# Kernel tuning notes

Hardware: AMD Instinct MI355X
Metric: run time of the kernel (lower is better)

The kernel has to match this reference:

```python
import jax, jax.numpy as jnp
import numpy as np

M_MARGIN = 0.5
SCALE = 64.0
COS_M = float(np.cos(M_MARGIN))
SIN_M = float(np.sin(M_MARGIN))
TH = -COS_M
MM = SIN_M * M_MARGIN
NUM_CLASSES = 100000
IN_FEATURES = 512
BATCH = 512


def setup_inputs() -> dict:
    key = jax.random.key(0)
    k1, k2, k3 = jax.random.split(key, 3)
    x = jax.random.normal(k1, (BATCH, IN_FEATURES), dtype=jnp.float32)
    y = jax.random.randint(k2, (BATCH,), 0, NUM_CLASSES, dtype=jnp.int64 if jax.config.jax_enable_x64 else jnp.int32)
    # xavier_uniform-like init for weight [num_classes, in_features]
    limit = float(np.sqrt(6.0 / (NUM_CLASSES + IN_FEATURES)))
    weight = jax.random.uniform(k3, (NUM_CLASSES, IN_FEATURES), minval=-limit, maxval=limit, dtype=jnp.float32)
    return {"x": x, "y": y, "weight": weight}


def _l2_normalize(v, axis=-1, eps=1e-12):
    # matches F.normalize(p=2): v / max(||v||, eps)
    n = jnp.sqrt(jnp.sum(v * v, axis=axis, keepdims=True))
    return v / jnp.maximum(n, eps)


def reference(x, y, weight):
    # cosine logits: [B, C]
    xn = _l2_normalize(x)
    wn = _l2_normalize(weight)
    cos = jnp.einsum('bd,cd->bc', xn, wn)
    sin = jnp.sqrt(jnp.clip(1.0 - cos * cos, 0.0))
    cos_w_margin = cos * COS_M - sin * SIN_M
    cos_w_margin = jnp.where(cos > TH, cos_w_margin, cos - MM)
    ohe = jax.nn.one_hot(y, NUM_CLASSES, dtype=jnp.bool_)
    logit = jnp.where(ohe, cos_w_margin, cos) * SCALE
    # cross entropy, mean reduction
    logp = jax.nn.log_softmax(logit, axis=-1)
    nll = -jnp.take_along_axis(logp, y[:, None], axis=-1)[:, 0]
    return jnp.mean(nll)
```

## Files before the change

kernel.cpp:

```cpp
#include <hip/hip_runtime.h>
#include <hip/hip_bf16.h>
#include <cstdint>
#include <cstddef>

#define C_CLS   100000
#define D_FEAT  512
#define B_ROWS  512

#define COSM 0.8775825618903728f
#define SINM 0.479425538604203f
#define TH_  (-0.8775825618903728f)
#define MM_  0.2397127693021015f

typedef __bf16 bf16x8 __attribute__((ext_vector_type(8)));
typedef __bf16 bf16x4 __attribute__((ext_vector_type(4)));
typedef float  f32x4  __attribute__((ext_vector_type(4)));

typedef __attribute__((address_space(3))) void lds_void;
typedef const __attribute__((address_space(1))) void g_void;

__device__ __forceinline__ void async_copy16(const void* g, void* l) {
    __builtin_amdgcn_global_load_lds((g_void*)g, (lds_void*)l, 16, 0, 0);
}

__global__ void k_xnorm(const float* __restrict__ x, __bf16* __restrict__ xn,
                        float* __restrict__ row_sum, float* __restrict__ tlogit) {
    const int row  = blockIdx.x;
    const int lane = threadIdx.x;
    const f32x4* p = (const f32x4*)(x + (size_t)row * D_FEAT);
    f32x4 a = p[lane];
    f32x4 b = p[lane + 64];
    float s = a[0]*a[0] + a[1]*a[1] + a[2]*a[2] + a[3]*a[3]
            + b[0]*b[0] + b[1]*b[1] + b[2]*b[2] + b[3]*b[3];
    #pragma unroll
    for (int m = 32; m >= 1; m >>= 1) s += __shfl_xor(s, m, 64);
    const float inv = 1.0f / fmaxf(sqrtf(s), 1e-12f);
    bf16x4 o0 = { (__bf16)(a[0]*inv), (__bf16)(a[1]*inv), (__bf16)(a[2]*inv), (__bf16)(a[3]*inv) };
    bf16x4 o1 = { (__bf16)(b[0]*inv), (__bf16)(b[1]*inv), (__bf16)(b[2]*inv), (__bf16)(b[3]*inv) };
    *(bf16x4*)(xn + (size_t)row * D_FEAT + lane * 4)       = o0;
    *(bf16x4*)(xn + (size_t)row * D_FEAT + 256 + lane * 4) = o1;
    if (lane == 0) { row_sum[row] = 0.0f; tlogit[row] = 0.0f; }
}

__global__ void k_wnorm(const float* __restrict__ w, float* __restrict__ inv_wn) {
    const int row  = blockIdx.x * 4 + (threadIdx.x >> 6);
    const int lane = threadIdx.x & 63;
    if (row >= C_CLS) return;
    const f32x4* p = (const f32x4*)(w + (size_t)row * D_FEAT);
    f32x4 a = p[lane];
    f32x4 b = p[lane + 64];
    float s = a[0]*a[0] + a[1]*a[1] + a[2]*a[2] + a[3]*a[3]
            + b[0]*b[0] + b[1]*b[1] + b[2]*b[2] + b[3]*b[3];
    #pragma unroll
    for (int m = 32; m >= 1; m >>= 1) s += __shfl_xor(s, m, 64);
    if (lane == 0) inv_wn[row] = 1.0f / fmaxf(sqrtf(s), 1e-12f);
}

__global__ __launch_bounds__(256, 2) void k_gemm(
        const __bf16* __restrict__ xn, const float* __restrict__ w,
        const float* __restrict__ inv_wn, const int* __restrict__ y,
        float* __restrict__ row_sum, float* __restrict__ tlogit) {

    __shared__ __align__(16) __bf16 As[4 * 128 * 8];
    __shared__ __align__(16) float  Bs[4 * 128 * 8];
    __shared__ int ys[128];

    const int tid = threadIdx.x;
    const int bm  = blockIdx.x & 3;
    const int bn  = blockIdx.x >> 2;

    if (tid < 128) ys[tid] = y[bm * 128 + tid];

    const int wave = tid >> 6;
    const int lane = tid & 63;
    const int wm   = wave >> 1;
    const int wn   = wave & 1;
    const int quad = lane >> 4;
    const int l15  = lane & 15;

    f32x4 acc[4][4];
    #pragma unroll
    for (int i = 0; i < 4; ++i)
        #pragma unroll
        for (int j = 0; j < 4; ++j) acc[i][j] = (f32x4){0.f, 0.f, 0.f, 0.f};

    for (int kt = 0; kt < 16; ++kt) {
        const int k0 = kt * 32;
        #pragma unroll
        for (int i = 0; i < 2; ++i) {
            const int c  = tid + i * 256;
            const int qc = c >> 7, rc = c & 127;
            const __bf16* g = xn + (size_t)(bm * 128 + rc) * D_FEAT + k0 + qc * 8;
            async_copy16(g, &As[(size_t)c * 8]);
        }
        #pragma unroll
        for (int i = 0; i < 4; ++i) {
            const int c  = tid + i * 256;
            const int qc = c >> 8, rc = (c >> 1) & 127, hc = c & 1;
            int grow = bn * 128 + rc; if (grow > C_CLS - 1) grow = C_CLS - 1;
            const float* g = w + (size_t)grow * D_FEAT + k0 + qc * 8 + hc * 4;
            async_copy16(g, &Bs[(size_t)c * 4]);
        }
        __syncthreads();

        bf16x8 af[4];
        #pragma unroll
        for (int mi = 0; mi < 4; ++mi) {
            const int r = wm * 64 + mi * 16 + l15;
            af[mi] = *(const bf16x8*)&As[(size_t)(quad * 128 + r) * 8];
        }
        bf16x8 bfr[4];
        #pragma unroll
        for (int ni = 0; ni < 4; ++ni) {
            const int r = wn * 64 + ni * 16 + l15;
            const float* bp = &Bs[(size_t)(quad * 128 + r) * 8];
            f32x4 b0 = *(const f32x4*)bp;
            f32x4 b1 = *(const f32x4*)(bp + 4);
            bf16x8 t;
            t[0] = (__bf16)b0[0]; t[1] = (__bf16)b0[1]; t[2] = (__bf16)b0[2]; t[3] = (__bf16)b0[3];
            t[4] = (__bf16)b1[0]; t[5] = (__bf16)b1[1]; t[6] = (__bf16)b1[2]; t[7] = (__bf16)b1[3];
            bfr[ni] = t;
        }
        #pragma unroll
        for (int mi = 0; mi < 4; ++mi)
            #pragma unroll
            for (int ni = 0; ni < 4; ++ni)
                acc[mi][ni] = __builtin_amdgcn_mfma_f32_16x16x32_bf16(af[mi], bfr[ni], acc[mi][ni], 0, 0, 0);
        __syncthreads();
    }

    #pragma unroll
    for (int mi = 0; mi < 4; ++mi) {
        float rs[4] = {0.f, 0.f, 0.f, 0.f};
        #pragma unroll
        for (int ni = 0; ni < 4; ++ni) {
            const int lcol = wn * 64 + ni * 16 + l15;
            const int gcol = bn * 128 + lcol;
            const bool colv = (gcol < C_CLS);
            const float invw = inv_wn[colv ? gcol : (C_CLS - 1)];
            #pragma unroll
            for (int reg = 0; reg < 4; ++reg) {
                const int lrow = wm * 64 + mi * 16 + quad * 4 + reg;
                const float cosv = acc[mi][ni][reg] * invw;
                const float sinv = sqrtf(fmaxf(1.0f - cosv * cosv, 0.0f));
                const float phi  = (cosv > TH_) ? (cosv * COSM - sinv * SINM) : (cosv - MM_);
                const bool ist   = colv && (gcol == ys[lrow]);
                const float logit = 64.0f * (ist ? phi : cosv);
                if (ist) tlogit[bm * 128 + lrow] = logit;
                rs[reg] += colv ? __expf(logit - 64.0f) : 0.0f;
            }
        }
        #pragma unroll
        for (int reg = 0; reg < 4; ++reg) {
            float v = rs[reg];
            v += __shfl_xor(v, 8, 64);
            v += __shfl_xor(v, 4, 64);
            v += __shfl_xor(v, 2, 64);
            v += __shfl_xor(v, 1, 64);
            if (l15 == 0) {
                const int lrow = wm * 64 + mi * 16 + quad * 4 + reg;
                atomicAdd(&row_sum[bm * 128 + lrow], v);
            }
        }
    }
}

__global__ void k_final(const float* __restrict__ row_sum, const float* __restrict__ tlogit,
                        float* __restrict__ out) {
    const int t = threadIdx.x;
    float v = logf(row_sum[t]) + 64.0f - tlogit[t];
    #pragma unroll
    for (int m = 32; m >= 1; m >>= 1) v += __shfl_xor(v, m, 64);
    __shared__ float partial[8];
    if ((t & 63) == 0) partial[t >> 6] = v;
    __syncthreads();
    if (t == 0) {
        float s = 0.f;
        #pragma unroll
        for (int i = 0; i < 8; ++i) s += partial[i];
        out[0] = s * (1.0f / 512.0f);
    }
}

extern "C" void kernel_launch(void* const* d_in, const int* in_sizes, int n_in,
                              void* d_out, int out_size, void* d_ws, size_t ws_size,
                              hipStream_t stream) {
    const float* x = (const float*)d_in[0];
    const int*   y = (const int*)d_in[1];
    const float* w = (const float*)d_in[2];

    char* ws = (char*)d_ws;
    __bf16* xn      = (__bf16*)ws;
    float*  inv_wn  = (float*)(ws + 524288);
    float*  row_sum = (float*)(ws + 524288 + 400000);
    float*  tlogit  = (float*)(ws + 524288 + 400000 + 2048);
    float*  out     = (float*)d_out;

    hipLaunchKernelGGL(k_xnorm, dim3(512), dim3(64), 0, stream, x, xn, row_sum, tlogit);
    hipLaunchKernelGGL(k_wnorm, dim3(25000), dim3(256), 0, stream, w, inv_wn);
    hipLaunchKernelGGL(k_gemm, dim3(4 * 782), dim3(256), 0, stream, xn, w, inv_wn, y, row_sum, tlogit);
    hipLaunchKernelGGL(k_final, dim3(1), dim3(512), 0, stream, row_sum, tlogit, out);
}
```

Before: 501.6 us.

## Fuse weight-norm into GEMM, double-buffer loads, replace atomics with partial sums

Removes the separate weight-normalization kernel by accumulating each column's sum of squares from the fp32 tiles the GEMM already loads into LDS. This saves a full extra pass over the 200MB weight matrix. The GEMM main loop is now double-buffered: the next tile's async loads are issued with explicit vmcnt waits and barriers, so memory overlaps MFMA work. Per-row atomic adds are replaced by per-block partial sums written to a workspace, which a wider final kernel reduces. Occupancy is raised to 3 blocks per CU, at the cost of more LDS and register pressure.

```diff
diff --git a/kernel.cpp b/kernel.cpp
--- a/kernel.cpp
+++ b/kernel.cpp
@@ -6,6 +6,7 @@
 #define C_CLS   100000
 #define D_FEAT  512
 #define B_ROWS  512
+#define NBN     782
 
 #define COSM 0.8775825618903728f
 #define SINM 0.479425538604203f
@@ -24,9 +25,10 @@
 }
 
 __global__ void k_xnorm(const float* __restrict__ x, __bf16* __restrict__ xn,
-                        float* __restrict__ row_sum, float* __restrict__ tlogit) {
+                        float* __restrict__ out) {
     const int row  = blockIdx.x;
     const int lane = threadIdx.x;
+    if (row == 0 && lane == 0) out[0] = 0.0f;
     const f32x4* p = (const f32x4*)(x + (size_t)row * D_FEAT);
     f32x4 a = p[lane];
     f32x4 b = p[lane + 64];
@@ -39,31 +41,17 @@
     bf16x4 o1 = { (__bf16)(b[0]*inv), (__bf16)(b[1]*inv), (__bf16)(b[2]*inv), (__bf16)(b[3]*inv) };
     *(bf16x4*)(xn + (size_t)row * D_FEAT + lane * 4)       = o0;
     *(bf16x4*)(xn + (size_t)row * D_FEAT + 256 + lane * 4) = o1;
-    if (lane == 0) { row_sum[row] = 0.0f; tlogit[row] = 0.0f; }
-}
-
-__global__ void k_wnorm(const float* __restrict__ w, float* __restrict__ inv_wn) {
-    const int row  = blockIdx.x * 4 + (threadIdx.x >> 6);
-    const int lane = threadIdx.x & 63;
-    if (row >= C_CLS) return;
-    const f32x4* p = (const f32x4*)(w + (size_t)row * D_FEAT);
-    f32x4 a = p[lane];
-    f32x4 b = p[lane + 64];
-    float s = a[0]*a[0] + a[1]*a[1] + a[2]*a[2] + a[3]*a[3]
-            + b[0]*b[0] + b[1]*b[1] + b[2]*b[2] + b[3]*b[3];
-    #pragma unroll
-    for (int m = 32; m >= 1; m >>= 1) s += __shfl_xor(s, m, 64);
-    if (lane == 0) inv_wn[row] = 1.0f / fmaxf(sqrtf(s), 1e-12f);
-}
-
-__global__ __launch_bounds__(256, 2) void k_gemm(
+}
+
+__global__ __launch_bounds__(256, 3) void k_gemm(
         const __bf16* __restrict__ xn, const float* __restrict__ w,
-        const float* __restrict__ inv_wn, const int* __restrict__ y,
-        float* __restrict__ row_sum, float* __restrict__ tlogit) {
-
-    __shared__ __align__(16) __bf16 As[4 * 128 * 8];
-    __shared__ __align__(16) float  Bs[4 * 128 * 8];
-    __shared__ int ys[128];
+        const int* __restrict__ y,
+        float* __restrict__ psum, float* __restrict__ tlogit) {
+
+    __shared__ __align__(16) __bf16 As[2][4096];
+    __shared__ __align__(16) float  Bs[2][4096];
+    __shared__ int   ys[128];
+    __shared__ float red[2][128];
 
     const int tid = threadIdx.x;
     const int bm  = blockIdx.x & 3;
@@ -83,50 +71,76 @@
     for (int i = 0; i < 4; ++i)
         #pragma unroll
         for (int j = 0; j < 4; ++j) acc[i][j] = (f32x4){0.f, 0.f, 0.f, 0.f};
-
+    float ssq[4] = {0.f, 0.f, 0.f, 0.f};
+
+    #define STAGE(s, kt_) do {                                                          \
+        const int k0_ = (kt_) * 32;                                                     \
+        _Pragma("unroll")                                                               \
+        for (int i_ = 0; i_ < 2; ++i_) {                                                \
+            const int c_ = tid + i_ * 256;                                              \
+            const int qc_ = c_ >> 7, rc_ = c_ & 127;                                    \
+            async_copy16(xn + (size_t)(bm * 128 + rc_) * D_FEAT + k0_ + qc_ * 8,        \
+                         &As[s][c_ * 8]);                                               \
+        }                                                                               \
+        _Pragma("unroll")                                                               \
+        for (int i_ = 0; i_ < 4; ++i_) {                                                \
+            const int c_ = tid + i_ * 256;                                              \
+            const int qc_ = c_ >> 8, rc_ = (c_ >> 1) & 127, hc_ = c_ & 1;               \
+            int grow_ = bn * 128 + rc_; if (grow_ > C_CLS - 1) grow_ = C_CLS - 1;       \
+            async_copy16(w + (size_t)grow_ * D_FEAT + k0_ + qc_ * 8 + hc_ * 4,          \
+                         &Bs[s][c_ * 4]);                                               \
+        }                                                                               \
+    } while (0)
+
+    STAGE(0, 0);
+    STAGE(1, 1);
+
+    #pragma unroll
     for (int kt = 0; kt < 16; ++kt) {
-        const int k0 = kt * 32;
-        #pragma unroll
-        for (int i = 0; i < 2; ++i) {
-            const int c  = tid + i * 256;
-            const int qc = c >> 7, rc = c & 127;
-            const __bf16* g = xn + (size_t)(bm * 128 + rc) * D_FEAT + k0 + qc * 8;
-            async_copy16(g, &As[(size_t)c * 8]);
-        }
-        #pragma unroll
-        for (int i = 0; i < 4; ++i) {
-            const int c  = tid + i * 256;
-            const int qc = c >> 8, rc = (c >> 1) & 127, hc = c & 1;
-            int grow = bn * 128 + rc; if (grow > C_CLS - 1) grow = C_CLS - 1;
-            const float* g = w + (size_t)grow * D_FEAT + k0 + qc * 8 + hc * 4;
-            async_copy16(g, &Bs[(size_t)c * 4]);
-        }
-        __syncthreads();
+        const int cur = kt & 1;
+
+        if (kt < 15) asm volatile("s_waitcnt vmcnt(6)" ::: "memory");
+        else         asm volatile("s_waitcnt vmcnt(0)" ::: "memory");
+        __builtin_amdgcn_s_barrier();
 
         bf16x8 af[4];
         #pragma unroll
-        for (int mi = 0; mi < 4; ++mi) {
-            const int r = wm * 64 + mi * 16 + l15;
-            af[mi] = *(const bf16x8*)&As[(size_t)(quad * 128 + r) * 8];
-        }
+        for (int mi = 0; mi < 4; ++mi)
+            af[mi] = *(const bf16x8*)&As[cur][(quad * 128 + wm * 64 + mi * 16 + l15) * 8];
+
         bf16x8 bfr[4];
         #pragma unroll
         for (int ni = 0; ni < 4; ++ni) {
-            const int r = wn * 64 + ni * 16 + l15;
-            const float* bp = &Bs[(size_t)(quad * 128 + r) * 8];
+            const float* bp = &Bs[cur][(quad * 128 + wn * 64 + ni * 16 + l15) * 8];
             f32x4 b0 = *(const f32x4*)bp;
             f32x4 b1 = *(const f32x4*)(bp + 4);
+            ssq[ni] += b0[0]*b0[0] + b0[1]*b0[1] + b0[2]*b0[2] + b0[3]*b0[3]
+                     + b1[0]*b1[0] + b1[1]*b1[1] + b1[2]*b1[2] + b1[3]*b1[3];
             bf16x8 t;
             t[0] = (__bf16)b0[0]; t[1] = (__bf16)b0[1]; t[2] = (__bf16)b0[2]; t[3] = (__bf16)b0[3];
             t[4] = (__bf16)b1[0]; t[5] = (__bf16)b1[1]; t[6] = (__bf16)b1[2]; t[7] = (__bf16)b1[3];
             bfr[ni] = t;
         }
+
+        asm volatile("s_waitcnt lgkmcnt(0)" ::: "memory");
+        __builtin_amdgcn_s_barrier();
+        if (kt < 14) STAGE(cur, kt + 2);
+
         #pragma unroll
         for (int mi = 0; mi < 4; ++mi)
             #pragma unroll
             for (int ni = 0; ni < 4; ++ni)
                 acc[mi][ni] = __builtin_amdgcn_mfma_f32_16x16x32_bf16(af[mi], bfr[ni], acc[mi][ni], 0, 0, 0);
-        __syncthreads();
+    }
+    #undef STAGE
+
+    float invw[4];
+    #pragma unroll
+    for (int ni = 0; ni < 4; ++ni) {
+        float s = ssq[ni];
+        s += __shfl_xor(s, 16, 64);
+        s += __shfl_xor(s, 32, 64);
+        invw[ni] = 1.0f / fmaxf(sqrtf(s), 1e-12f);
     }
 
     #pragma unroll
@@ -134,14 +148,12 @@
         float rs[4] = {0.f, 0.f, 0.f, 0.f};
         #pragma unroll
         for (int ni = 0; ni < 4; ++ni) {
-            const int lcol = wn * 64 + ni * 16 + l15;
-            const int gcol = bn * 128 + lcol;
+            const int gcol = bn * 128 + wn * 64 + ni * 16 + l15;
             const bool colv = (gcol < C_CLS);
-            const float invw = inv_wn[colv ? gcol : (C_CLS - 1)];
             #pragma unroll
             for (int reg = 0; reg < 4; ++reg) {
                 const int lrow = wm * 64 + mi * 16 + quad * 4 + reg;
-                const float cosv = acc[mi][ni][reg] * invw;
+                const float cosv = acc[mi][ni][reg] * invw[ni];
                 const float sinv = sqrtf(fmaxf(1.0f - cosv * cosv, 0.0f));
                 const float phi  = (cosv > TH_) ? (cosv * COSM - sinv * SINM) : (cosv - MM_);
                 const bool ist   = colv && (gcol == ys[lrow]);
@@ -157,28 +169,28 @@
             v += __shfl_xor(v, 4, 64);
             v += __shfl_xor(v, 2, 64);
             v += __shfl_xor(v, 1, 64);
-            if (l15 == 0) {
-                const int lrow = wm * 64 + mi * 16 + quad * 4 + reg;
-                atomicAdd(&row_sum[bm * 128 + lrow], v);
-            }
+            if (l15 == 0) red[wn][wm * 64 + mi * 16 + quad * 4 + reg] = v;
         }
     }
-}
-
-__global__ void k_final(const float* __restrict__ row_sum, const float* __restrict__ tlogit,
+    __syncthreads();
+    if (tid < 128) {
+        const float v = red[0][tid] + red[1][tid];
+        psum[(size_t)(bm * 128 + tid) * NBN + bn] = v;
+    }
+}
+
+__global__ void k_final(const float* __restrict__ psum, const float* __restrict__ tlogit,
                         float* __restrict__ out) {
-    const int t = threadIdx.x;
-    float v = logf(row_sum[t]) + 64.0f - tlogit[t];
-    #pragma unroll
-    for (int m = 32; m >= 1; m >>= 1) v += __shfl_xor(v, m, 64);
-    __shared__ float partial[8];
-    if ((t & 63) == 0) partial[t >> 6] = v;
-    __syncthreads();
-    if (t == 0) {
-        float s = 0.f;
-        #pragma unroll
-        for (int i = 0; i < 8; ++i) s += partial[i];
-        out[0] = s * (1.0f / 512.0f);
+    const int row = blockIdx.x * 4 + (threadIdx.x >> 6);
+    const int l   = threadIdx.x & 63;
+    const float* p = psum + (size_t)row * NBN;
+    float s = 0.0f;
+    for (int i = l; i < NBN; i += 64) s += p[i];
+    #pragma unroll
+    for (int m = 32; m >= 1; m >>= 1) s += __shfl_xor(s, m, 64);
+    if (l == 0) {
+        const float loss = logf(s) + 64.0f - tlogit[row];
+        atomicAdd(out, loss * (1.0f / 512.0f));
     }
 }
 
@@ -190,14 +202,12 @@
     const float* w = (const float*)d_in[2];
 
     char* ws = (char*)d_ws;
-    __bf16* xn      = (__bf16*)ws;
-    float*  inv_wn  = (float*)(ws + 524288);
-    float*  row_sum = (float*)(ws + 524288 + 400000);
-    float*  tlogit  = (float*)(ws + 524288 + 400000 + 2048);
-    float*  out     = (float*)d_out;
-
-    hipLaunchKernelGGL(k_xnorm, dim3(512), dim3(64), 0, stream, x, xn, row_sum, tlogit);
-    hipLaunchKernelGGL(k_wnorm, dim3(25000), dim3(256), 0, stream, w, inv_wn);
-    hipLaunchKernelGGL(k_gemm, dim3(4 * 782), dim3(256), 0, stream, xn, w, inv_wn, y, row_sum, tlogit);
-    hipLaunchKernelGGL(k_final, dim3(1), dim3(512), 0, stream, row_sum, tlogit, out);
-}
+    __bf16* xn     = (__bf16*)ws;
+    float*  psum   = (float*)(ws + 524288);
+    float*  tlogit = (float*)(ws + 524288 + 1601536);
+    float*  out    = (float*)d_out;
+
+    hipLaunchKernelGGL(k_xnorm, dim3(512), dim3(64), 0, stream, x, xn, out);
+    hipLaunchKernelGGL(k_gemm, dim3(4 * NBN), dim3(256), 0, stream, xn, w, y, psum, tlogit);
+    hipLaunchKernelGGL(k_final, dim3(128), dim3(256), 0, stream, psum, tlogit, out);
+}
```

Result: faster. 423.1 us (-15.7%).
